# Kernel tuning notes

Measured on AMD Instinct MI355X. Metric: run time of the kernel, lower is better.

The kernel has to match this reference:

```python
import jax, jax.numpy as jnp
import numpy as np

# DeformConv1d config (matches init_kwargs)
K = 3          # kernel_size
DIL = 1        # dilation
STRIDE = 1
PAD = DIL * (K - 1)  # 'same' total padding = 2 -> (1,1) reflect


def setup_inputs() -> dict:
    key = jax.random.key(0)
    k1, k2, k3, k4 = jax.random.split(key, 4)
    B, C, L = 16, 64, 8192
    O = 64
    x = jax.random.normal(k1, (B, C, L), dtype=jnp.float32)
    offsets = jax.random.normal(k2, (B, 1, L, K), dtype=jnp.float32)
    weight = jax.random.normal(k3, (O, C, K), dtype=jnp.float32) * (1.0 / np.sqrt(C * K))
    bias = jax.random.normal(k4, (O,), dtype=jnp.float32) * 0.01
    return {"x": x, "offsets": offsets, "weight": weight, "bias": bias}


def _deform_conv1d(x, offsets, weight, bias):
    # reflect 'same' padding: left = PAD//2, right = PAD - PAD//2
    left = PAD // 2
    x_pad = jnp.pad(x, ((0, 0), (0, 0), (left, PAD - left)), mode="reflect")
    B, C, Lp = x_pad.shape
    OL = offsets.shape[-2]
    dt = x.dtype

    dilated = (jnp.arange(K, dtype=dt) * DIL)          # [K] = [0, d, ..., d(K-1)]
    t0 = (jnp.arange(OL, dtype=dt) * STRIDE)[:, None]  # [OL, 1]

    # sampling positions T: [B, G, OL, K], constrained to kernel receptive field
    T = t0 + dilated + offsets
    T = jnp.maximum(T, t0)
    T = jnp.minimum(T, t0 + dilated[-1])

    # integer lower neighbors (no grad through floor); clamp so U+1 is valid
    U = jnp.clip(jnp.floor(T).astype(jnp.int32), 0, Lp - 2)  # [B, G, OL, K]

    # gather both neighbors along length axis (broadcast offset group -> C)
    idx = jnp.broadcast_to(U, (B, C, OL, K)).reshape(B, C, OL * K)
    x0 = jnp.take_along_axis(x_pad, idx, axis=2).reshape(B, C, OL, K)
    x1 = jnp.take_along_axis(x_pad, idx + 1, axis=2).reshape(B, C, OL, K)

    # linear interpolation weights G = max(0, 1 - |U - T|)
    Uf = U.astype(dt)
    w0 = jnp.maximum(0.0, 1.0 - jnp.abs(Uf - T))        # [B, G, OL, K]
    w1 = jnp.maximum(0.0, 1.0 - jnp.abs(Uf + 1.0 - T))
    sampled = w0 * x0 + w1 * x1                          # [B, C, OL, K]

    # conv1d(weight, stride=K) on flattened [B, C, OL*K] == per-position contraction
    out = jnp.einsum("bcok,fck->bfo", sampled, weight) + bias[None, :, None]
    return out


def reference(x, offsets, weight, bias):
    return _deform_conv1d(x, offsets, weight, bias)
```

## Files before the change

### kernel.cpp

```cpp
#include <hip/hip_runtime.h>
#include <stdint.h>

#define BB   16
#define CC   64
#define LL   8192
#define OO   64
#define KK   3
#define TT   64
#define XSW  72
#define SW   200

typedef __attribute__((ext_vector_type(8))) short short8;
typedef __attribute__((ext_vector_type(4))) float float4_t;

__device__ __forceinline__ ushort f2bf(float f) {
    uint32_t u = __float_as_uint(f);
    return (ushort)((u + 0x7FFFu + ((u >> 16) & 1u)) >> 16);
}
__device__ __forceinline__ float bf2f(ushort h) {
    return __uint_as_float(((uint32_t)h) << 16);
}

__global__ void wt_prep(const float* __restrict__ w, ushort* __restrict__ wt) {
    int idx = blockIdx.x * 256 + threadIdx.x;
    if (idx < OO * CC * KK) {
        int f = idx / (CC * KK);
        int rem = idx - f * (CC * KK);
        int c = rem / KK;
        int k = rem - c * KK;
        wt[f * (KK * CC) + k * CC + c] = f2bf(w[idx]);
    }
}

__global__ __launch_bounds__(256, 2) void deform_main(
    const float* __restrict__ x, const float* __restrict__ offs,
    const ushort* __restrict__ wt, const float* __restrict__ bias,
    float* __restrict__ out) {

    __shared__ ushort xs[67 * XSW];
    __shared__ ushort S[TT * SW];
    __shared__ ushort Wt[OO * SW];
    __shared__ int    Ul[TT * KK];
    __shared__ float  W0s[TT * KK], W1s[TT * KK];

    const int tid  = threadIdx.x;
    const int bb   = blockIdx.x >> 7;
    const int tile = blockIdx.x & 127;
    const int ts   = tile * TT;

    {
        const uint4* src = (const uint4*)wt;
        #pragma unroll
        for (int i = 0; i < 6; i++) {
            int idx = tid + i * 256;
            int e0  = idx * 8;
            int row = e0 / 192;
            int col = e0 - row * 192;
            *(uint4*)&Wt[row * SW + col] = src[idx];
        }
    }

    {
        const float* xb = x + (size_t)bb * (CC * LL);
        #pragma unroll
        for (int i = 0; i < 17; i++) {
            int idx = tid + i * 256;
            if (idx < 64 * 67) {
                int c = idx / 67;
                int p = idx - c * 67;
                int j = ts + p - 1;
                if (j < 0) j = -j;
                if (j >= LL) j = 2 * LL - 2 - j;
                xs[p * XSW + c] = f2bf(xb[c * LL + j]);
            }
        }
    }

    if (tid < TT * KK) {
        int n = tid / 3;
        int k = tid - n * 3;
        float off = offs[((size_t)bb * LL + ts + n) * 3 + k];
        float t0  = (float)(ts + n);
        float T   = t0 + (float)k + off;
        T = fmaxf(T, t0);
        T = fminf(T, t0 + 2.0f);
        int U = (int)floorf(T);
        if (U > LL) U = LL;
        float Uf = (float)U;
        float w0 = fmaxf(0.0f, 1.0f - fabsf(Uf - T));
        float w1 = fmaxf(0.0f, 1.0f - fabsf(Uf + 1.0f - T));
        Ul[tid]  = U - ts;
        W0s[tid] = w0;
        W1s[tid] = w1;
    }
    __syncthreads();

    #pragma unroll
    for (int i = 0; i < 6; i++) {
        int tau = tid + i * 256;
        int g   = tau & 7;
        int nk  = tau >> 3;
        int n   = nk / 3;
        int k   = nk - n * 3;
        int u   = Ul[nk];
        float w0 = W0s[nk], w1 = W1s[nk];
        int c0  = g * 8;
        union { uint4 v; ushort u16[8]; } r0, r1;
        r0.v = *(const uint4*)&xs[u * XSW + c0];
        r1.v = *(const uint4*)&xs[(u + 1) * XSW + c0];
        uint32_t pk[4];
        #pragma unroll
        for (int j = 0; j < 4; j++) {
            float v0 = w0 * bf2f(r0.u16[2 * j])     + w1 * bf2f(r1.u16[2 * j]);
            float v1 = w0 * bf2f(r0.u16[2 * j + 1]) + w1 * bf2f(r1.u16[2 * j + 1]);
            pk[j] = (uint32_t)f2bf(v0) | ((uint32_t)f2bf(v1) << 16);
        }
        uint4 ov;
        ov.x = pk[0]; ov.y = pk[1]; ov.z = pk[2]; ov.w = pk[3];
        *(uint4*)&S[n * SW + k * 64 + c0] = ov;
    }
    __syncthreads();

    const int lane = tid & 63;
    const int wv   = tid >> 6;
    const int lr   = lane & 15;
    const int q    = lane >> 4;
    float4_t acc0 = {0.f, 0.f, 0.f, 0.f};
    float4_t acc1 = acc0, acc2 = acc0, acc3 = acc0;

    #pragma unroll
    for (int kk = 0; kk < 6; kk++) {
        int k0 = kk * 32 + q * 8;
        short8 a  = *(const short8*)&Wt[(wv * 16 + lr) * SW + k0];
        short8 b0 = *(const short8*)&S[(0 * 16 + lr) * SW + k0];
        short8 b1 = *(const short8*)&S[(1 * 16 + lr) * SW + k0];
        short8 b2 = *(const short8*)&S[(2 * 16 + lr) * SW + k0];
        short8 b3 = *(const short8*)&S[(3 * 16 + lr) * SW + k0];
        acc0 = __builtin_amdgcn_mfma_f32_16x16x32_bf16(a, b0, acc0, 0, 0, 0);
        acc1 = __builtin_amdgcn_mfma_f32_16x16x32_bf16(a, b1, acc1, 0, 0, 0);
        acc2 = __builtin_amdgcn_mfma_f32_16x16x32_bf16(a, b2, acc2, 0, 0, 0);
        acc3 = __builtin_amdgcn_mfma_f32_16x16x32_bf16(a, b3, acc3, 0, 0, 0);
    }

    const int f0 = wv * 16 + q * 4;
    float4_t bv = *(const float4_t*)&bias[f0];
    float* ob = out + ((size_t)bb * OO + f0) * LL + ts;
    #pragma unroll
    for (int r = 0; r < 4; r++) {
        float* orow = ob + (size_t)r * LL;
        orow[ 0 + lr] = acc0[r] + bv[r];
        orow[16 + lr] = acc1[r] + bv[r];
        orow[32 + lr] = acc2[r] + bv[r];
        orow[48 + lr] = acc3[r] + bv[r];
    }
}

extern "C" void kernel_launch(void* const* d_in, const int* in_sizes, int n_in,
                              void* d_out, int out_size, void* d_ws, size_t ws_size,
                              hipStream_t stream) {
    const float* x    = (const float*)d_in[0];
    const float* offs = (const float*)d_in[1];
    const float* w    = (const float*)d_in[2];
    const float* bias = (const float*)d_in[3];
    float* out = (float*)d_out;
    ushort* wt = (ushort*)d_ws;

    hipLaunchKernelGGL(wt_prep, dim3((OO * CC * KK + 255) / 256), dim3(256), 0, stream, w, wt);
    hipLaunchKernelGGL(deform_main, dim3(BB * (LL / TT)), dim3(256), 0, stream,
                       x, offs, wt, bias, out);
}
```

Before: 107.5 us.

## Fuse weight prep into main kernel, alias LDS buffer, raise occupancy

Drops the separate weight-conversion kernel. Each block now reads the fp32 weights directly, converts them to bf16 and transposes them into shared memory. The A fragments are preloaded into registers, so the weight buffer can be reused for the sampled tile, which roughly halves LDS use and allows raising launch bounds to 4 blocks per SM. This removes one kernel launch and improves occupancy. In exchange, every block repeats the weight conversion with scalar scattered LDS writes and holds more registers, and one extra barrier is added.

New measurement: 104.1 us. -3.2%, faster.

```diff
diff --git a/kernel.cpp b/kernel.cpp
--- a/kernel.cpp
+++ b/kernel.cpp
@@ -21,25 +21,13 @@
     return __uint_as_float(((uint32_t)h) << 16);
 }
 
-__global__ void wt_prep(const float* __restrict__ w, ushort* __restrict__ wt) {
-    int idx = blockIdx.x * 256 + threadIdx.x;
-    if (idx < OO * CC * KK) {
-        int f = idx / (CC * KK);
-        int rem = idx - f * (CC * KK);
-        int c = rem / KK;
-        int k = rem - c * KK;
-        wt[f * (KK * CC) + k * CC + c] = f2bf(w[idx]);
-    }
-}
-
-__global__ __launch_bounds__(256, 2) void deform_main(
+__global__ __launch_bounds__(256, 4) void deform_main(
     const float* __restrict__ x, const float* __restrict__ offs,
-    const ushort* __restrict__ wt, const float* __restrict__ bias,
+    const float* __restrict__ w, const float* __restrict__ bias,
     float* __restrict__ out) {
 
+    __shared__ ushort buf[TT * SW];
     __shared__ ushort xs[67 * XSW];
-    __shared__ ushort S[TT * SW];
-    __shared__ ushort Wt[OO * SW];
     __shared__ int    Ul[TT * KK];
     __shared__ float  W0s[TT * KK], W1s[TT * KK];
 
@@ -49,14 +37,20 @@
     const int ts   = tile * TT;
 
     {
-        const uint4* src = (const uint4*)wt;
+        const float4_t* src = (const float4_t*)w;
         #pragma unroll
-        for (int i = 0; i < 6; i++) {
-            int idx = tid + i * 256;
-            int e0  = idx * 8;
-            int row = e0 / 192;
-            int col = e0 - row * 192;
-            *(uint4*)&Wt[row * SW + col] = src[idx];
+        for (int i = 0; i < 12; i++) {
+            int idx4 = tid + i * 256;
+            float4_t v = src[idx4];
+            int f  = idx4 / 48;
+            int e0 = (idx4 - f * 48) * 4;
+            #pragma unroll
+            for (int j = 0; j < 4; j++) {
+                int e = e0 + j;
+                int c = e / 3;
+                int k = e - c * 3;
+                buf[f * SW + k * 64 + c] = f2bf(v[j]);
+            }
         }
     }
 
@@ -87,12 +81,21 @@
         int U = (int)floorf(T);
         if (U > LL) U = LL;
         float Uf = (float)U;
-        float w0 = fmaxf(0.0f, 1.0f - fabsf(Uf - T));
-        float w1 = fmaxf(0.0f, 1.0f - fabsf(Uf + 1.0f - T));
         Ul[tid]  = U - ts;
-        W0s[tid] = w0;
-        W1s[tid] = w1;
+        W0s[tid] = fmaxf(0.0f, 1.0f - fabsf(Uf - T));
+        W1s[tid] = fmaxf(0.0f, 1.0f - fabsf(Uf + 1.0f - T));
     }
+    __syncthreads();
+
+    const int lane = tid & 63;
+    const int wv   = tid >> 6;
+    const int lr   = lane & 15;
+    const int q    = lane >> 4;
+
+    short8 a[6];
+    #pragma unroll
+    for (int kk = 0; kk < 6; kk++)
+        a[kk] = *(const short8*)&buf[(wv * 16 + lr) * SW + kk * 32 + q * 8];
     __syncthreads();
 
     #pragma unroll
@@ -117,29 +120,24 @@
         }
         uint4 ov;
         ov.x = pk[0]; ov.y = pk[1]; ov.z = pk[2]; ov.w = pk[3];
-        *(uint4*)&S[n * SW + k * 64 + c0] = ov;
+        *(uint4*)&buf[n * SW + k * 64 + c0] = ov;
     }
     __syncthreads();
 
-    const int lane = tid & 63;
-    const int wv   = tid >> 6;
-    const int lr   = lane & 15;
-    const int q    = lane >> 4;
     float4_t acc0 = {0.f, 0.f, 0.f, 0.f};
     float4_t acc1 = acc0, acc2 = acc0, acc3 = acc0;
 
     #pragma unroll
     for (int kk = 0; kk < 6; kk++) {
         int k0 = kk * 32 + q * 8;
-        short8 a  = *(const short8*)&Wt[(wv * 16 + lr) * SW + k0];
-        short8 b0 = *(const short8*)&S[(0 * 16 + lr) * SW + k0];
-        short8 b1 = *(const short8*)&S[(1 * 16 + lr) * SW + k0];
-        short8 b2 = *(const short8*)&S[(2 * 16 + lr) * SW + k0];
-        short8 b3 = *(const short8*)&S[(3 * 16 + lr) * SW + k0];
-        acc0 = __builtin_amdgcn_mfma_f32_16x16x32_bf16(a, b0, acc0, 0, 0, 0);
-        acc1 = __builtin_amdgcn_mfma_f32_16x16x32_bf16(a, b1, acc1, 0, 0, 0);
-        acc2 = __builtin_amdgcn_mfma_f32_16x16x32_bf16(a, b2, acc2, 0, 0, 0);
-        acc3 = __builtin_amdgcn_mfma_f32_16x16x32_bf16(a, b3, acc3, 0, 0, 0);
+        short8 b0 = *(const short8*)&buf[( 0 + lr) * SW + k0];
+        short8 b1 = *(const short8*)&buf[(16 + lr) * SW + k0];
+        short8 b2 = *(const short8*)&buf[(32 + lr) * SW + k0];
+        short8 b3 = *(const short8*)&buf[(48 + lr) * SW + k0];
+        acc0 = __builtin_amdgcn_mfma_f32_16x16x32_bf16(a[kk], b0, acc0, 0, 0, 0);
+        acc1 = __builtin_amdgcn_mfma_f32_16x16x32_bf16(a[kk], b1, acc1, 0, 0, 0);
+        acc2 = __builtin_amdgcn_mfma_f32_16x16x32_bf16(a[kk], b2, acc2, 0, 0, 0);
+        acc3 = __builtin_amdgcn_mfma_f32_16x16x32_bf16(a[kk], b3, acc3, 0, 0, 0);
     }
 
     const int f0 = wv * 16 + q * 4;
@@ -158,14 +156,13 @@
 extern "C" void kernel_launch(void* const* d_in, const int* in_sizes, int n_in,
                               void* d_out, int out_size, void* d_ws, size_t ws_size,
                               hipStream_t stream) {
+    (void)d_ws; (void)ws_size;
     const float* x    = (const float*)d_in[0];
     const float* offs = (const float*)d_in[1];
     const float* w    = (const float*)d_in[2];
     const float* bias = (const float*)d_in[3];
     float* out = (float*)d_out;
-    ushort* wt = (ushort*)d_ws;
 
-    hipLaunchKernelGGL(wt_prep, dim3((OO * CC * KK + 255) / 256), dim3(256), 0, stream, w, wt);
     hipLaunchKernelGGL(deform_main, dim3(BB * (LL / TT)), dim3(256), 0, stream,
-                       x, offs, wt, bias, out);
+                       x, offs, w, bias, out);
 }
```
